# Performance work log

Measured on AMD Instinct MI355X. Metric: run time of the kernel, lower is better.

Reference implementation:

```python
import jax, jax.numpy as jnp
import numpy as np

B, LQ, LK, H, DK, DV, E = 4, 1024, 1024, 12, 64, 768, 768
TOPK = 64
TEMP = 0.5
NEG = -10000.0


def setup_inputs() -> dict:
    key = jax.random.key(0)
    ks = jax.random.split(key, 10)
    s = 0.02  # weight init scale
    return {
        "q": jax.random.normal(ks[0], (B, LQ, E), jnp.float32),
        "k": jax.random.normal(ks[1], (B, LK, E), jnp.float32),
        "v": jax.random.normal(ks[2], (B, LK, DV), jnp.float32),
        "qpos": jnp.zeros((B, LQ), jnp.int32),
        "kpos": jnp.zeros((B, LK), jnp.int32),
        "qk_mask": jax.random.normal(ks[3], (B, 1, LQ, LK), jnp.float32) * 0.1,
        "k_mask": jax.random.normal(ks[4], (B, 1, LK, 1), jnp.float32) * 0.1,
        "post_softmax_mask": (jax.random.uniform(ks[5], (B, 1, LQ, LK)) > 0.1).astype(jnp.float32),
        "w_qs": jax.random.normal(ks[6], (E, H * DK), jnp.float32) * s,
        "w_ks": jax.random.normal(ks[7], (E, H * DK), jnp.float32) * s,
        "w_vs": jax.random.normal(ks[8], (DV, H * DV), jnp.float32) * s,
        "fc": jax.random.normal(ks[9], (H * DV, DV), jnp.float32) * s,
    }


def reference(q, k, v, qpos, kpos, qk_mask, k_mask, post_softmax_mask, w_qs, w_ks, w_vs, fc):
    residual = v
    # project and split heads: [b, len, h, d] -> [b, h, len, d]
    qh = (q @ w_qs).reshape(B, LQ, H, DK).transpose(0, 2, 1, 3)
    kh = (k @ w_ks).reshape(B, LK, H, DK).transpose(0, 2, 1, 3)
    vh = (v @ w_vs).reshape(B, LK, H, DV).transpose(0, 2, 1, 3)

    # scaled dot-product scores [b, h, lq, lk]
    attn = jnp.einsum('bhqd,bhkd->bhqk', qh / np.float32(np.sqrt(DK)), kh)
    attn = attn + qk_mask                              # additive qk mask
    attn = attn + jnp.squeeze(k_mask, -1)[:, :, None, :]  # additive key mask

    # topk sparsification: keep top-k scores, fill rest with -10000
    topk_vals, topk_idx = jax.lax.top_k(attn, TOPK)
    attn = jnp.put_along_axis(jnp.full_like(attn, NEG), topk_idx, topk_vals,
                              axis=-1, inplace=False)

    # temperature + stable softmax in fp32
    attn = attn / max(TEMP, 1e-6)
    attn = jax.nn.softmax(attn.astype(jnp.float32), axis=-1).astype(v.dtype)

    # post-softmax multiplicative mask + renorm (renorm_post_mask=True)
    attn = attn * post_softmax_mask
    attn = attn / jnp.maximum(attn.sum(axis=-1, keepdims=True), 1e-6)

    # straight-through argmax hardening (use_argmax=True)
    hard = jax.nn.one_hot(jnp.argmax(attn, axis=-1), LK, dtype=attn.dtype)
    attn = hard - jax.lax.stop_gradient(attn) + attn

    # attend, merge heads, output projection + residual (dropout=0)
    head_output = jnp.einsum('bhqk,bhkd->bhqd', attn, vh)
    output = head_output.transpose(0, 2, 1, 3).reshape(B, LQ, H * DV) @ fc
    output = output + residual
    return (output, attn)
```

## Files before the change

### kernel.cpp

```cpp
#include <hip/hip_runtime.h>

constexpr int NB  = 4;
constexpr int NH  = 12;
constexpr int SEQ = 1024;
constexpr int DKd = 64;
constexpr int DVd = 768;
constexpr int Ed  = 768;
constexpr int HVd = 9216;

typedef float f32x4 __attribute__((ext_vector_type(4)));
typedef short s16x8 __attribute__((ext_vector_type(8)));

__device__ __forceinline__ unsigned short f2bf(float f) {
  unsigned int u = __builtin_bit_cast(unsigned int, f);
  u += 0x7fffu + ((u >> 16) & 1u);
  return (unsigned short)(u >> 16);
}

__device__ __forceinline__ float bf2f_lo(unsigned int u) {
  return __builtin_bit_cast(float, u << 16);
}
__device__ __forceinline__ float bf2f_hi(unsigned int u) {
  return __builtin_bit_cast(float, u & 0xffff0000u);
}

__device__ __forceinline__ f32x4 mfma_bf16_16x16x32(s16x8 a, s16x8 b, f32x4 c) {
  asm("v_mfma_f32_16x16x32_bf16 %0, %1, %2, %0" : "+v"(c) : "v"(a), "v"(b));
  return c;
}

#define GLOAD16(g, l)                                                          \
  __builtin_amdgcn_global_load_lds(                                            \
      (const __attribute__((address_space(1))) unsigned int*)(g),              \
      (__attribute__((address_space(3))) unsigned int*)(l), 16, 0, 0)

__global__ __launch_bounds__(256)
void cvt_bf16_kernel(const float* __restrict__ v, unsigned short* __restrict__ Vbf, int n4) {
  int i = blockIdx.x * 256 + threadIdx.x;
  const int stride = gridDim.x * 256;
  for (; i < n4; i += stride) {
    const f32x4 x = *(const f32x4*)&v[(size_t)i * 4];
    uint2 u;
    u.x = (unsigned)f2bf(x[0]) | ((unsigned)f2bf(x[1]) << 16);
    u.y = (unsigned)f2bf(x[2]) | ((unsigned)f2bf(x[3]) << 16);
    *(uint2*)&Vbf[(size_t)i * 4] = u;
  }
}

__global__ __launch_bounds__(256)
void maskprep_kernel(const float* __restrict__ qk, const float* __restrict__ km,
                     const float* __restrict__ pm, float* __restrict__ ms) {
  const int i = blockIdx.x * 256 + threadIdx.x;
  const int kk4 = i & 255;
  const int b = i >> 18;
  const f32x4 qv = *(const f32x4*)&qk[(size_t)i * 4];
  const f32x4 pv = *(const f32x4*)&pm[(size_t)i * 4];
  const f32x4 kv = *(const f32x4*)&km[b * SEQ + kk4 * 4];
  f32x4 o;
#pragma unroll
  for (int c = 0; c < 4; c++) o[c] = pv[c] > 0.f ? qv[c] + kv[c] : -3.0e38f;
  *(f32x4*)&ms[(size_t)i * 4] = o;
}

__global__ __launch_bounds__(256)
void qkproj_kernel(const float* __restrict__ q, const float* __restrict__ k,
                   const float* __restrict__ w_qs, const float* __restrict__ w_ks,
                   float* __restrict__ qh, float* __restrict__ kh) {
  const float* A  = blockIdx.z ? k : q;
  const float* Bw = blockIdx.z ? w_ks : w_qs;
  float* C        = blockIdx.z ? kh : qh;
  __shared__ float As[16][128];
  __shared__ float Bs[16][64];
  const int tid = threadIdx.x;
  const int m0 = blockIdx.x * 128, n0 = blockIdx.y * 64;
  const int ty = tid >> 4, tx = tid & 15;
  const int arow = tid >> 1, akc = (tid & 1) * 8;
  const int bkr = tid >> 4, bnc = (tid & 15) * 4;

  float acc[8][4];
#pragma unroll
  for (int i = 0; i < 8; i++)
#pragma unroll
    for (int j = 0; j < 4; j++) acc[i][j] = 0.f;

  for (int k0 = 0; k0 < 768; k0 += 16) {
    const f32x4 av0 = *(const f32x4*)&A[(size_t)(m0 + arow) * 768 + k0 + akc];
    const f32x4 av1 = *(const f32x4*)&A[(size_t)(m0 + arow) * 768 + k0 + akc + 4];
    const f32x4 bv  = *(const f32x4*)&Bw[(size_t)(k0 + bkr) * 768 + n0 + bnc];
    __syncthreads();
#pragma unroll
    for (int c = 0; c < 4; c++) {
      As[akc + c][arow]     = av0[c];
      As[akc + 4 + c][arow] = av1[c];
    }
    *(f32x4*)&Bs[bkr][bnc] = bv;
    __syncthreads();
#pragma unroll
    for (int kk = 0; kk < 16; kk++) {
      const f32x4 a0 = *(const f32x4*)&As[kk][ty * 8];
      const f32x4 a1 = *(const f32x4*)&As[kk][ty * 8 + 4];
      const f32x4 b  = *(const f32x4*)&Bs[kk][tx * 4];
#pragma unroll
      for (int i = 0; i < 4; i++)
#pragma unroll
        for (int j = 0; j < 4; j++) {
          acc[i][j]     += a0[i] * b[j];
          acc[i + 4][j] += a1[i] * b[j];
        }
    }
  }
#pragma unroll
  for (int i = 0; i < 8; i++) {
    f32x4 o;
#pragma unroll
    for (int j = 0; j < 4; j++) o[j] = acc[i][j];
    *(f32x4*)&C[(size_t)(m0 + ty * 8 + i) * 768 + n0 + tx * 4] = o;
  }
}

__global__ __launch_bounds__(256)
void score_argmax_kernel(const float* __restrict__ qh, const float* __restrict__ kh,
                         const float* __restrict__ ms, float2* __restrict__ partials) {
  __shared__ float msS[64][128];
  __shared__ float QsT[64][64];
  __shared__ float KsT[64][128];
  const int b  = blockIdx.z;
  const int q0 = blockIdx.y * 64;
  const int k0 = blockIdx.x * 128;
  const int tid = threadIdx.x;
  const int ty = tid >> 4, tx = tid & 15;

  {
    const int row = tid >> 2, cc = (tid & 3) * 32;
    const float* src = ms + (size_t)(b * SEQ + q0 + row) * SEQ + k0 + cc;
#pragma unroll
    for (int i = 0; i < 8; i++)
      *(f32x4*)&msS[row][cc + 4 * i] = *(const f32x4*)&src[4 * i];
  }

  const int qr = tid >> 2, qdc = (tid & 3) * 16;
  const int kr = tid >> 1, kdc = (tid & 1) * 32;
  const float* qbase = qh + (size_t)(b * SEQ + q0 + qr) * Ed + qdc;
  const float* kbase = kh + (size_t)(b * SEQ + k0 + kr) * Ed + kdc;
  const int kg0 = k0 + tx * 8;

  for (int h = 0; h < NH; h++) {
    __syncthreads();
#pragma unroll
    for (int j = 0; j < 4; j++) {
      const f32x4 qv = *(const f32x4*)&qbase[h * 64 + 4 * j];
#pragma unroll
      for (int c = 0; c < 4; c++) QsT[qdc + 4 * j + c][qr] = qv[c];
    }
#pragma unroll
    for (int j = 0; j < 8; j++) {
      const f32x4 kv = *(const f32x4*)&kbase[h * 64 + 4 * j];
#pragma unroll
      for (int c = 0; c < 4; c++) KsT[kdc + 4 * j + c][kr] = kv[c];
    }
    __syncthreads();

    float acc[4][8];
#pragma unroll
    for (int i = 0; i < 4; i++)
#pragma unroll
      for (int j = 0; j < 8; j++) acc[i][j] = 0.f;

#pragma unroll 8
    for (int kk = 0; kk < 64; kk++) {
      const f32x4 qf  = *(const f32x4*)&QsT[kk][ty * 4];
      const f32x4 kf0 = *(const f32x4*)&KsT[kk][tx * 8];
      const f32x4 kf1 = *(const f32x4*)&KsT[kk][tx * 8 + 4];
#pragma unroll
      for (int i = 0; i < 4; i++)
#pragma unroll
        for (int j = 0; j < 4; j++) {
          acc[i][j]     += qf[i] * kf0[j];
          acc[i][j + 4] += qf[i] * kf1[j];
        }
    }

#pragma unroll
    for (int i = 0; i < 4; i++) {
      const int qg = q0 + ty * 4 + i;
      const f32x4 m0v = *(const f32x4*)&msS[ty * 4 + i][tx * 8];
      const f32x4 m1v = *(const f32x4*)&msS[ty * 4 + i][tx * 8 + 4];
      float bv = -3.0e38f;
      int bi = 0;
#pragma unroll
      for (int j = 0; j < 4; j++) {
        const float s = acc[i][j] * 0.125f + m0v[j];
        if (s > bv) { bv = s; bi = kg0 + j; }
      }
#pragma unroll
      for (int j = 0; j < 4; j++) {
        const float s = acc[i][4 + j] * 0.125f + m1v[j];
        if (s > bv) { bv = s; bi = kg0 + 4 + j; }
      }
#pragma unroll
      for (int off = 1; off < 16; off <<= 1) {
        const float ov = __shfl_xor(bv, off);
        const int   oi = __shfl_xor(bi, off);
        if (ov > bv || (ov == bv && oi < bi)) { bv = ov; bi = oi; }
      }
      if (tx == 0)
        partials[(size_t)((b * NH + h) * SEQ + qg) * 8 + blockIdx.x] =
            make_float2(bv, __int_as_float(bi));
    }
  }
}

__global__ __launch_bounds__(256)
void argmax_reduce_kernel(const float2* __restrict__ partials, int* __restrict__ kmaxp) {
  const int t = blockIdx.x * 256 + threadIdx.x;
  if (t >= NB * NH * SEQ) return;
  const float2* p = partials + (size_t)t * 8;
  float bv = -3.0e38f;
  int bi = 0;
#pragma unroll
  for (int i = 0; i < 8; i++) {
    const float vv = p[i].x;
    const int ii = __float_as_int(p[i].y);
    if (vv > bv) { bv = vv; bi = ii; }
  }
  kmaxp[t] = bi;
}

__global__ __launch_bounds__(256)
void wvfc_gemm_kernel(const float* __restrict__ wvs, const float* __restrict__ fcw,
                      unsigned short* __restrict__ MstbT) {
  __shared__ unsigned short As[128][72];
  __shared__ unsigned short Bs[128][72];
  const int tid = threadIdx.x;
  const int h = blockIdx.z;
  const int m0 = blockIdx.x * 128, n0 = blockIdx.y * 128;
  const int wid = tid >> 6, lane = tid & 63;
  const int wr = (wid >> 1) * 64, wc = (wid & 1) * 64;
  const int lm = lane & 15, lq = lane >> 4;
  const int ar = tid >> 1, acb = (tid & 1) * 32;
  const int br = tid >> 2, bnb = (tid & 3) * 32;

  f32x4 acc[4][4];
#pragma unroll
  for (int m = 0; m < 4; m++)
#pragma unroll
    for (int n = 0; n < 4; n++)
#pragma unroll
      for (int r = 0; r < 4; r++) acc[m][n][r] = 0.f;

  for (int k0 = 0; k0 < 768; k0 += 64) {
    const float* asrc = wvs + (size_t)(m0 + ar) * HVd + h * 768 + k0 + acb;
    const float* bsrc = fcw + (size_t)(h * 768 + k0 + br) * 768 + n0 + bnb;
    f32x4 a4[8], b4[8];
#pragma unroll
    for (int i = 0; i < 8; i++) a4[i] = *(const f32x4*)&asrc[4 * i];
#pragma unroll
    for (int i = 0; i < 8; i++) b4[i] = *(const f32x4*)&bsrc[4 * i];
    __syncthreads();
#pragma unroll
    for (int i = 0; i < 4; i++) {
      s16x8 pk;
#pragma unroll
      for (int j = 0; j < 8; j++) pk[j] = (short)f2bf(a4[2 * i + (j >> 2)][j & 3]);
      *(s16x8*)&As[ar][acb + 8 * i] = pk;
    }
#pragma unroll
    for (int i = 0; i < 8; i++)
#pragma unroll
      for (int c = 0; c < 4; c++) Bs[bnb + 4 * i + c][br] = f2bf(b4[i][c]);
    __syncthreads();
#pragma unroll
    for (int ks = 0; ks < 2; ks++) {
      s16x8 af[4], bfr[4];
#pragma unroll
      for (int m = 0; m < 4; m++)
        af[m] = *(const s16x8*)&As[wr + m * 16 + lm][ks * 32 + lq * 8];
#pragma unroll
      for (int n = 0; n < 4; n++)
        bfr[n] = *(const s16x8*)&Bs[wc + n * 16 + lm][ks * 32 + lq * 8];
#pragma unroll
      for (int m = 0; m < 4; m++)
#pragma unroll
        for (int n = 0; n < 4; n++)
          acc[m][n] = mfma_bf16_16x16x32(af[m], bfr[n], acc[m][n]);
    }
  }
  asm volatile("s_nop 7\n\ts_nop 7");
#pragma unroll
  for (int m = 0; m < 4; m++)
#pragma unroll
    for (int n = 0; n < 4; n++) {
      const int grow0 = m0 + wr + m * 16 + lq * 4;
      const int gcol  = n0 + wc + n * 16 + lm;
      uint2 u;
      u.x = (unsigned)f2bf(acc[m][n][0]) | ((unsigned)f2bf(acc[m][n][1]) << 16);
      u.y = (unsigned)f2bf(acc[m][n][2]) | ((unsigned)f2bf(acc[m][n][3]) << 16);
      *(uint2*)&MstbT[(size_t)(h * 768 + gcol) * 768 + grow0] = u;
    }
}

__global__ __launch_bounds__(256)
void ugemm_kernel(const unsigned short* __restrict__ Vbf,
                  const unsigned short* __restrict__ MstbT,
                  unsigned short* __restrict__ U, int h0) {
  __shared__ unsigned short As[128 * 64];
  __shared__ unsigned short Bs[128 * 64];
  const int tid = threadIdx.x;
  const int h = h0 + blockIdx.z;
  const int bx = (int)blockIdx.x;
  const int sx = ((bx & 7) << 2) | (bx >> 3);
  const int m0 = sx * 128, n0 = blockIdx.y * 128;
  const int wid = tid >> 6, lane = tid & 63;
  const int wr = (wid >> 1) * 64, wc = (wid & 1) * 64;
  const int lm = lane & 15, lq = lane >> 4;
  const int srow = tid >> 3, scol = (tid & 7) * 8;
  const int ldst = (tid >> 6) * 512;

  const unsigned short* asrc = Vbf + (size_t)(m0 + srow) * 768 + scol;
  const unsigned short* bsrc = MstbT + (size_t)(h * 768 + n0 + srow) * 768 + scol;

  f32x4 acc[4][4];
#pragma unroll
  for (int m = 0; m < 4; m++)
#pragma unroll
    for (int n = 0; n < 4; n++)
#pragma unroll
      for (int r = 0; r < 4; r++) acc[m][n][r] = 0.f;

  for (int k0 = 0; k0 < 768; k0 += 64) {
#pragma unroll
    for (int j = 0; j < 4; j++)
      GLOAD16(asrc + (size_t)j * 32 * 768 + k0, &As[j * 2048 + ldst]);
#pragma unroll
    for (int j = 0; j < 4; j++)
      GLOAD16(bsrc + (size_t)j * 32 * 768 + k0, &Bs[j * 2048 + ldst]);
    __syncthreads();
#pragma unroll
    for (int ks = 0; ks < 2; ks++) {
      s16x8 af[4], bfr[4];
#pragma unroll
      for (int m = 0; m < 4; m++)
        af[m] = *(const s16x8*)&As[(wr + m * 16 + lm) * 64 + ks * 32 + lq * 8];
#pragma unroll
      for (int n = 0; n < 4; n++)
        bfr[n] = *(const s16x8*)&Bs[(wc + n * 16 + lm) * 64 + ks * 32 + lq * 8];
#pragma unroll
      for (int m = 0; m < 4; m++)
#pragma unroll
        for (int n = 0; n < 4; n++)
          acc[m][n] = mfma_bf16_16x16x32(af[m], bfr[n], acc[m][n]);
    }
    __syncthreads();
  }
  asm volatile("s_nop 7\n\ts_nop 7");
  const size_t urow0 = (size_t)blockIdx.z * 4096;
#pragma unroll
  for (int m = 0; m < 4; m++)
#pragma unroll
    for (int r = 0; r < 4; r++) {
      const int row = m0 + wr + m * 16 + lq * 4 + r;
      uint2 u;
      u.x = (unsigned)f2bf(acc[m][0][r]) | ((unsigned)f2bf(acc[m][1][r]) << 16);
      u.y = (unsigned)f2bf(acc[m][2][r]) | ((unsigned)f2bf(acc[m][3][r]) << 16);
      *(uint2*)&U[(urow0 + row) * 768 + n0 + wc + lm * 4] = u;
    }
}

__global__ __launch_bounds__(192)
void gathersum_kernel(const unsigned short* __restrict__ U, const int* __restrict__ kmaxp,
                      const float* __restrict__ v, float* __restrict__ out0,
                      int h0, int nhg) {
  const int row = blockIdx.x;
  const int b = row >> 10, q = row & 1023;
  const int t = threadIdx.x;
  float a0 = 0.f, a1 = 0.f, a2 = 0.f, a3 = 0.f;
  for (int hg = 0; hg < nhg; hg++) {
    const int g = kmaxp[((b * NH + h0 + hg) << 10) + q];
    const uint2 u = *(const uint2*)&U[((size_t)hg * 4096 + (b << 10) + g) * 768 + t * 4];
    a0 += bf2f_lo(u.x);
    a1 += bf2f_hi(u.x);
    a2 += bf2f_lo(u.y);
    a3 += bf2f_hi(u.y);
  }
  const int chunk = t >> 4, lmm = t & 15;
  const size_t ob = (size_t)row * 768 + chunk * 64 + lmm;
  if (h0 == 0) {
    out0[ob +  0] = a0 + v[ob +  0];
    out0[ob + 16] = a1 + v[ob + 16];
    out0[ob + 32] = a2 + v[ob + 32];
    out0[ob + 48] = a3 + v[ob + 48];
  } else {
    out0[ob +  0] += a0;
    out0[ob + 16] += a1;
    out0[ob + 32] += a2;
    out0[ob + 48] += a3;
  }
}

__global__ void onehot_kernel(const int* __restrict__ kmaxp, f32x4* __restrict__ attn, int n4) {
  int i = blockIdx.x * blockDim.x + threadIdx.x;
  const int stride = gridDim.x * blockDim.x;
  for (; i < n4; i += stride) {
    const int row = i >> 8;
    const int c0 = (i & 255) * 4;
    const int km = kmaxp[row];
    f32x4 o;
#pragma unroll
    for (int c = 0; c < 4; c++) o[c] = (c0 + c == km) ? 1.0f : 0.0f;
    attn[i] = o;
  }
}

extern "C" void kernel_launch(void* const* d_in, const int* in_sizes, int n_in,
                              void* d_out, int out_size, void* d_ws, size_t ws_size,
                              hipStream_t stream) {
  (void)in_sizes; (void)n_in; (void)out_size;
  const float* q       = (const float*)d_in[0];
  const float* k       = (const float*)d_in[1];
  const float* v       = (const float*)d_in[2];
  const float* qk_mask = (const float*)d_in[5];
  const float* k_mask  = (const float*)d_in[6];
  const float* pmask   = (const float*)d_in[7];
  const float* w_qs    = (const float*)d_in[8];
  const float* w_ks    = (const float*)d_in[9];
  const float* w_vs    = (const float*)d_in[10];
  const float* fc      = (const float*)d_in[11];

  float* out0 = (float*)d_out;
  float* attn = out0 + (size_t)NB * SEQ * DVd;

  char* ws = (char*)d_ws;
  unsigned short* MstbT = (unsigned short*)ws;
  unsigned short* Vbf   = (unsigned short*)(ws + 14155776);
  float* msbuf          = (float*)ws;
  int* kmaxp            = (int*)(ws + 20447232);
  char* ureg            = ws + 20643840;
  unsigned short* U     = (unsigned short*)ureg;
  float* qh             = (float*)ureg;
  float* kh             = (float*)(ureg + 12582912);
  float2* partials      = (float2*)(ureg + 25165824);

  const bool big = ws_size >= (size_t)96141312;

  maskprep_kernel<<<dim3(4096), 256, 0, stream>>>(qk_mask, k_mask, pmask, msbuf);

  qkproj_kernel<<<dim3(32, 12, 2), 256, 0, stream>>>(q, k, w_qs, w_ks, qh, kh);

  score_argmax_kernel<<<dim3(8, 16, NB), 256, 0, stream>>>(qh, kh, msbuf, partials);
  argmax_reduce_kernel<<<dim3((NB * NH * SEQ + 255) / 256), 256, 0, stream>>>(partials, kmaxp);

  cvt_bf16_kernel<<<dim3(3072), 256, 0, stream>>>(v, Vbf, NB * SEQ * DVd / 4);

  wvfc_gemm_kernel<<<dim3(6, 6, NH), 256, 0, stream>>>(w_vs, fc, MstbT);

  if (big) {
    ugemm_kernel<<<dim3(32, 6, 12), 256, 0, stream>>>(Vbf, MstbT, U, 0);
    gathersum_kernel<<<dim3(NB * SEQ), 192, 0, stream>>>(U, kmaxp, v, out0, 0, 12);
  } else {
    ugemm_kernel<<<dim3(32, 6, 6), 256, 0, stream>>>(Vbf, MstbT, U, 0);
    gathersum_kernel<<<dim3(NB * SEQ), 192, 0, stream>>>(U, kmaxp, v, out0, 0, 6);
    ugemm_kernel<<<dim3(32, 6, 6), 256, 0, stream>>>(Vbf, MstbT, U, 6);
    gathersum_kernel<<<dim3(NB * SEQ), 192, 0, stream>>>(U, kmaxp, v, out0, 6, 6);
  }

  onehot_kernel<<<dim3(2048), 256, 0, stream>>>(kmaxp, (f32x4*)attn,
                                                (int)((size_t)NB * NH * SEQ * SEQ / 4));
}
```

Measured before the change: 452.7 us.

## Use split-bf16 MFMA for QK projection, fuse mask prep, add argmax rescue

Replaces the fp32 scalar-FMA Q/K projection GEMM with a bf16 MFMA kernel that uses a hi/lo split, computing three products to approximate fp32 accuracy. This needs extra split and transpose kernels. The separate mask-prep pass is removed and its work is folded into score_argmax's shared-memory load, which avoids writing and re-reading a full-size mask buffer. The score kernel now tracks the top-2 candidates per row, and a rescue kernel recomputes near-tie rows in exact fp32 to guard argmax correctness against the reduced precision. The cost is extra launches and extra memory traffic for the split tensors.

```diff
diff --git a/kernel.cpp b/kernel.cpp
--- a/kernel.cpp
+++ b/kernel.cpp
@@ -16,12 +16,17 @@
   u += 0x7fffu + ((u >> 16) & 1u);
   return (unsigned short)(u >> 16);
 }
-
+__device__ __forceinline__ float bf2f(unsigned short h) {
+  return __builtin_bit_cast(float, (unsigned int)h << 16);
+}
 __device__ __forceinline__ float bf2f_lo(unsigned int u) {
   return __builtin_bit_cast(float, u << 16);
 }
 __device__ __forceinline__ float bf2f_hi(unsigned int u) {
   return __builtin_bit_cast(float, u & 0xffff0000u);
+}
+__device__ __forceinline__ bool better(float va, int ia, float vb, int ib) {
+  return va > vb || (va == vb && ia < ib);
 }
 
 __device__ __forceinline__ f32x4 mfma_bf16_16x16x32(s16x8 a, s16x8 b, f32x4 c) {
@@ -33,6 +38,312 @@
   __builtin_amdgcn_global_load_lds(                                            \
       (const __attribute__((address_space(1))) unsigned int*)(g),              \
       (__attribute__((address_space(3))) unsigned int*)(l), 16, 0, 0)
+
+__global__ __launch_bounds__(256)
+void split_qk_kernel(const float* __restrict__ q, const float* __restrict__ k,
+                     unsigned short* __restrict__ Qhi, unsigned short* __restrict__ Qlo,
+                     unsigned short* __restrict__ Khi, unsigned short* __restrict__ Klo,
+                     int n4) {
+  const float* src = blockIdx.z ? k : q;
+  unsigned short* hi = blockIdx.z ? Khi : Qhi;
+  unsigned short* lo = blockIdx.z ? Klo : Qlo;
+  int i = blockIdx.x * 256 + threadIdx.x;
+  const int stride = gridDim.x * 256;
+  for (; i < n4; i += stride) {
+    const f32x4 x = *(const f32x4*)&src[(size_t)i * 4];
+    unsigned short h[4], l[4];
+#pragma unroll
+    for (int c = 0; c < 4; c++) {
+      h[c] = f2bf(x[c]);
+      l[c] = f2bf(x[c] - bf2f(h[c]));
+    }
+    uint2 uh, ul;
+    uh.x = (unsigned)h[0] | ((unsigned)h[1] << 16);
+    uh.y = (unsigned)h[2] | ((unsigned)h[3] << 16);
+    ul.x = (unsigned)l[0] | ((unsigned)l[1] << 16);
+    ul.y = (unsigned)l[2] | ((unsigned)l[3] << 16);
+    *(uint2*)&hi[(size_t)i * 4] = uh;
+    *(uint2*)&lo[(size_t)i * 4] = ul;
+  }
+}
+
+__global__ __launch_bounds__(256)
+void split_wT_kernel(const float* __restrict__ w_qs, const float* __restrict__ w_ks,
+                     unsigned short* __restrict__ WqThi, unsigned short* __restrict__ WqTlo,
+                     unsigned short* __restrict__ WkThi, unsigned short* __restrict__ WkTlo) {
+  __shared__ float Ts[64][68];
+  const float* src = blockIdx.z ? w_ks : w_qs;
+  unsigned short* hi = blockIdx.z ? WkThi : WqThi;
+  unsigned short* lo = blockIdx.z ? WkTlo : WqTlo;
+  const int e0 = blockIdx.x * 64, n0 = blockIdx.y * 64;
+  const int tid = threadIdx.x;
+  const int row = tid >> 2, cc = (tid & 3) * 16;
+#pragma unroll
+  for (int j = 0; j < 4; j++)
+    *(f32x4*)&Ts[row][cc + 4 * j] = *(const f32x4*)&src[(size_t)(e0 + row) * 768 + n0 + cc + 4 * j];
+  __syncthreads();
+  const int r = tid >> 2, cs = (tid & 3) * 16;
+  s16x8 ph[2], pl[2];
+#pragma unroll
+  for (int j = 0; j < 16; j++) {
+    const float v = Ts[cs + j][r];
+    const unsigned short h = f2bf(v);
+    const unsigned short l = f2bf(v - bf2f(h));
+    ph[j >> 3][j & 7] = (short)h;
+    pl[j >> 3][j & 7] = (short)l;
+  }
+  const size_t ob = (size_t)(n0 + r) * 768 + e0 + cs;
+  *(s16x8*)&hi[ob] = ph[0];
+  *(s16x8*)&hi[ob + 8] = ph[1];
+  *(s16x8*)&lo[ob] = pl[0];
+  *(s16x8*)&lo[ob + 8] = pl[1];
+}
+
+__global__ __launch_bounds__(256)
+void qkproj_mfma_kernel(const unsigned short* __restrict__ Qhi, const unsigned short* __restrict__ Qlo,
+                        const unsigned short* __restrict__ Khi, const unsigned short* __restrict__ Klo,
+                        const unsigned short* __restrict__ WqThi, const unsigned short* __restrict__ WqTlo,
+                        const unsigned short* __restrict__ WkThi, const unsigned short* __restrict__ WkTlo,
+                        float* __restrict__ qh, float* __restrict__ kh) {
+  const unsigned short* Ahi = blockIdx.z ? Khi : Qhi;
+  const unsigned short* Alo = blockIdx.z ? Klo : Qlo;
+  const unsigned short* Bhi = blockIdx.z ? WkThi : WqThi;
+  const unsigned short* Blo = blockIdx.z ? WkTlo : WqTlo;
+  float* C = blockIdx.z ? kh : qh;
+  __shared__ unsigned short AhiS[128 * 64], AloS[128 * 64];
+  __shared__ unsigned short BhiS[64 * 64], BloS[64 * 64];
+  const int tid = threadIdx.x;
+  const int wid = tid >> 6, lane = tid & 63;
+  const int m0 = blockIdx.x * 128, n0 = blockIdx.y * 64;
+  const int wr = (wid >> 1) * 64, wc = (wid & 1) * 32;
+  const int lm = lane & 15, lq = lane >> 4;
+  const int srow = wid * 8 + (lane >> 3);
+  const int scols = (((lane & 7) * 16) ^ ((srow & 7) << 4)) >> 1;
+  const int ldst = wid * 512;
+  const int xs = (lm & 7) << 3;
+
+  const unsigned short* ahi0 = Ahi + (size_t)(m0 + srow) * 768 + scols;
+  const unsigned short* alo0 = Alo + (size_t)(m0 + srow) * 768 + scols;
+  const unsigned short* bhi0 = Bhi + (size_t)(n0 + srow) * 768 + scols;
+  const unsigned short* blo0 = Blo + (size_t)(n0 + srow) * 768 + scols;
+
+  f32x4 acc[4][2];
+#pragma unroll
+  for (int m = 0; m < 4; m++)
+#pragma unroll
+    for (int n = 0; n < 2; n++)
+#pragma unroll
+      for (int r = 0; r < 4; r++) acc[m][n][r] = 0.f;
+
+  for (int k0 = 0; k0 < 768; k0 += 64) {
+#pragma unroll
+    for (int j = 0; j < 4; j++) {
+      GLOAD16(ahi0 + (size_t)j * 32 * 768 + k0, &AhiS[j * 2048 + ldst]);
+      GLOAD16(alo0 + (size_t)j * 32 * 768 + k0, &AloS[j * 2048 + ldst]);
+    }
+#pragma unroll
+    for (int j = 0; j < 2; j++) {
+      GLOAD16(bhi0 + (size_t)j * 32 * 768 + k0, &BhiS[j * 2048 + ldst]);
+      GLOAD16(blo0 + (size_t)j * 32 * 768 + k0, &BloS[j * 2048 + ldst]);
+    }
+    __syncthreads();
+#pragma unroll
+    for (int ks = 0; ks < 2; ks++) {
+      const int kc = (ks * 32 + lq * 8) ^ xs;
+      s16x8 ah[4], al[4], bh[2], bl[2];
+#pragma unroll
+      for (int m = 0; m < 4; m++) {
+        ah[m] = *(const s16x8*)&AhiS[(wr + m * 16 + lm) * 64 + kc];
+        al[m] = *(const s16x8*)&AloS[(wr + m * 16 + lm) * 64 + kc];
+      }
+#pragma unroll
+      for (int n = 0; n < 2; n++) {
+        bh[n] = *(const s16x8*)&BhiS[(wc + n * 16 + lm) * 64 + kc];
+        bl[n] = *(const s16x8*)&BloS[(wc + n * 16 + lm) * 64 + kc];
+      }
+#pragma unroll
+      for (int m = 0; m < 4; m++)
+#pragma unroll
+        for (int n = 0; n < 2; n++) {
+          acc[m][n] = mfma_bf16_16x16x32(ah[m], bh[n], acc[m][n]);
+          acc[m][n] = mfma_bf16_16x16x32(al[m], bh[n], acc[m][n]);
+          acc[m][n] = mfma_bf16_16x16x32(ah[m], bl[n], acc[m][n]);
+        }
+    }
+    __syncthreads();
+  }
+  asm volatile("s_nop 7\n\ts_nop 7");
+#pragma unroll
+  for (int m = 0; m < 4; m++)
+#pragma unroll
+    for (int n = 0; n < 2; n++)
+#pragma unroll
+      for (int r = 0; r < 4; r++)
+        C[(size_t)(m0 + wr + m * 16 + lq * 4 + r) * 768 + n0 + wc + n * 16 + lm] =
+            acc[m][n][r];
+}
+
+__global__ __launch_bounds__(256)
+void score_argmax_kernel(const float* __restrict__ qh, const float* __restrict__ kh,
+                         const float* __restrict__ qkm, const float* __restrict__ km,
+                         const float* __restrict__ pm, float4* __restrict__ partials) {
+  __shared__ float msS[64][128];
+  __shared__ float QsT[64][64];
+  __shared__ float KsT[64][128];
+  const int b  = blockIdx.z;
+  const int q0 = blockIdx.y * 64;
+  const int k0 = blockIdx.x * 128;
+  const int tid = threadIdx.x;
+  const int ty = tid >> 4, tx = tid & 15;
+
+  {
+    const int row = tid >> 2, cc = (tid & 3) * 32;
+    const size_t base = (size_t)(b * SEQ + q0 + row) * SEQ + k0 + cc;
+#pragma unroll
+    for (int i = 0; i < 8; i++) {
+      const f32x4 qv = *(const f32x4*)&qkm[base + 4 * i];
+      const f32x4 pv = *(const f32x4*)&pm[base + 4 * i];
+      const f32x4 kv = *(const f32x4*)&km[b * SEQ + k0 + cc + 4 * i];
+      f32x4 o;
+#pragma unroll
+      for (int c = 0; c < 4; c++) o[c] = pv[c] > 0.f ? qv[c] + kv[c] : -3.0e38f;
+      *(f32x4*)&msS[row][cc + 4 * i] = o;
+    }
+  }
+
+  const int qr = tid >> 2, qdc = (tid & 3) * 16;
+  const int kr = tid >> 1, kdc = (tid & 1) * 32;
+  const float* qbase = qh + (size_t)(b * SEQ + q0 + qr) * Ed + qdc;
+  const float* kbase = kh + (size_t)(b * SEQ + k0 + kr) * Ed + kdc;
+  const int kg0 = k0 + tx * 8;
+
+  for (int h = 0; h < NH; h++) {
+    __syncthreads();
+#pragma unroll
+    for (int j = 0; j < 4; j++) {
+      const f32x4 qv = *(const f32x4*)&qbase[h * 64 + 4 * j];
+#pragma unroll
+      for (int c = 0; c < 4; c++) QsT[qdc + 4 * j + c][qr] = qv[c];
+    }
+#pragma unroll
+    for (int j = 0; j < 8; j++) {
+      const f32x4 kv = *(const f32x4*)&kbase[h * 64 + 4 * j];
+#pragma unroll
+      for (int c = 0; c < 4; c++) KsT[kdc + 4 * j + c][kr] = kv[c];
+    }
+    __syncthreads();
+
+    float acc[4][8];
+#pragma unroll
+    for (int i = 0; i < 4; i++)
+#pragma unroll
+      for (int j = 0; j < 8; j++) acc[i][j] = 0.f;
+
+#pragma unroll 8
+    for (int kk = 0; kk < 64; kk++) {
+      const f32x4 qf  = *(const f32x4*)&QsT[kk][ty * 4];
+      const f32x4 kf0 = *(const f32x4*)&KsT[kk][tx * 8];
+      const f32x4 kf1 = *(const f32x4*)&KsT[kk][tx * 8 + 4];
+#pragma unroll
+      for (int i = 0; i < 4; i++)
+#pragma unroll
+        for (int j = 0; j < 4; j++) {
+          acc[i][j]     += qf[i] * kf0[j];
+          acc[i][j + 4] += qf[i] * kf1[j];
+        }
+    }
+
+#pragma unroll
+    for (int i = 0; i < 4; i++) {
+      const int qg = q0 + ty * 4 + i;
+      const f32x4 m0v = *(const f32x4*)&msS[ty * 4 + i][tx * 8];
+      const f32x4 m1v = *(const f32x4*)&msS[ty * 4 + i][tx * 8 + 4];
+      float v1 = -3.0e38f, v2 = -3.0e38f;
+      int i1 = 0, i2 = 0;
+#pragma unroll
+      for (int j = 0; j < 8; j++) {
+        const float s = acc[i][j] * 0.125f + (j < 4 ? m0v[j & 3] : m1v[j & 3]);
+        const int idx = kg0 + j;
+        if (better(s, idx, v1, i1)) { v2 = v1; i2 = i1; v1 = s; i1 = idx; }
+        else if (better(s, idx, v2, i2)) { v2 = s; i2 = idx; }
+      }
+#pragma unroll
+      for (int off = 1; off < 16; off <<= 1) {
+        const float w1 = __shfl_xor(v1, off); const int j1 = __shfl_xor(i1, off);
+        const float w2 = __shfl_xor(v2, off); const int j2 = __shfl_xor(i2, off);
+        if (better(w1, j1, v1, i1)) {
+          if (better(v1, i1, w2, j2)) { v2 = v1; i2 = i1; } else { v2 = w2; i2 = j2; }
+          v1 = w1; i1 = j1;
+        } else if (better(w1, j1, v2, i2)) { v2 = w1; i2 = j1; }
+      }
+      if (tx == 0)
+        partials[(size_t)((b * NH + h) * SEQ + qg) * 8 + blockIdx.x] =
+            make_float4(v1, __int_as_float(i1), v2, __int_as_float(i2));
+    }
+  }
+}
+
+__global__ __launch_bounds__(256)
+void argmax_reduce_kernel(const float4* __restrict__ partials, int* __restrict__ kmaxp,
+                          float4* __restrict__ aux) {
+  const int t = blockIdx.x * 256 + threadIdx.x;
+  if (t >= NB * NH * SEQ) return;
+  const float4* p = partials + (size_t)t * 8;
+  float v1 = -3.0e38f, v2 = -3.0e38f;
+  int i1 = 0, i2 = 0;
+#pragma unroll
+  for (int i = 0; i < 8; i++) {
+    const float w1 = p[i].x; const int j1 = __float_as_int(p[i].y);
+    const float w2 = p[i].z; const int j2 = __float_as_int(p[i].w);
+    if (better(w1, j1, v1, i1)) {
+      if (better(v1, i1, w2, j2)) { v2 = v1; i2 = i1; } else { v2 = w2; i2 = j2; }
+      v1 = w1; i1 = j1;
+    } else if (better(w1, j1, v2, i2)) { v2 = w1; i2 = j1; }
+  }
+  kmaxp[t] = i1;
+  aux[t] = make_float4(v1, __int_as_float(i1), v2, __int_as_float(i2));
+}
+
+__global__ __launch_bounds__(256)
+void rescue_kernel(const float4* __restrict__ aux, const float* __restrict__ q,
+                   const float* __restrict__ k, const float* __restrict__ w_qs,
+                   const float* __restrict__ w_ks, const float* __restrict__ qkm,
+                   const float* __restrict__ km, const float* __restrict__ pm,
+                   int* __restrict__ kmaxp) {
+  const int row = blockIdx.x * 4 + (threadIdx.x >> 6);
+  const float4 a = aux[row];
+  if (a.x - a.z > 5e-4f) return;
+  const int i1 = __float_as_int(a.y), i2 = __float_as_int(a.w);
+  if (i1 == i2) return;
+  const int bh = row >> 10, qq = row & 1023;
+  const int b = bh / NH, h = bh % NH;
+  const int lane = threadIdx.x & 63;
+  const float* qr = q + (size_t)(b * SEQ + qq) * Ed;
+  const float* k1 = k + (size_t)(b * SEQ + i1) * Ed;
+  const float* k2 = k + (size_t)(b * SEQ + i2) * Ed;
+  const float* wq = w_qs + h * DKd + lane;
+  const float* wk = w_ks + h * DKd + lane;
+  float qd = 0.f, k1d = 0.f, k2d = 0.f;
+#pragma unroll 4
+  for (int e = 0; e < Ed; e++) {
+    const float wqe = wq[(size_t)e * 768];
+    const float wke = wk[(size_t)e * 768];
+    qd  += qr[e] * wqe;
+    k1d += k1[e] * wke;
+    k2d += k2[e] * wke;
+  }
+  float s1 = qd * k1d, s2 = qd * k2d;
+#pragma unroll
+  for (int off = 1; off < 64; off <<= 1) {
+    s1 += __shfl_xor(s1, off);
+    s2 += __shfl_xor(s2, off);
+  }
+  const size_t m1 = (size_t)(b * SEQ + qq) * SEQ + i1;
+  const size_t m2 = (size_t)(b * SEQ + qq) * SEQ + i2;
+  s1 = s1 * 0.125f + (pm[m1] > 0.f ? qkm[m1] + km[b * SEQ + i1] : -3.0e38f);
+  s2 = s2 * 0.125f + (pm[m2] > 0.f ? qkm[m2] + km[b * SEQ + i2] : -3.0e38f);
+  if (lane == 0) kmaxp[row] = better(s1, i1, s2, i2) ? i1 : i2;
+}
 
 __global__ __launch_bounds__(256)
 void cvt_bf16_kernel(const float* __restrict__ v, unsigned short* __restrict__ Vbf, int n4) {
@@ -45,185 +356,6 @@
     u.y = (unsigned)f2bf(x[2]) | ((unsigned)f2bf(x[3]) << 16);
     *(uint2*)&Vbf[(size_t)i * 4] = u;
   }
-}
-
-__global__ __launch_bounds__(256)
-void maskprep_kernel(const float* __restrict__ qk, const float* __restrict__ km,
-                     const float* __restrict__ pm, float* __restrict__ ms) {
-  const int i = blockIdx.x * 256 + threadIdx.x;
-  const int kk4 = i & 255;
-  const int b = i >> 18;
-  const f32x4 qv = *(const f32x4*)&qk[(size_t)i * 4];
-  const f32x4 pv = *(const f32x4*)&pm[(size_t)i * 4];
-  const f32x4 kv = *(const f32x4*)&km[b * SEQ + kk4 * 4];
-  f32x4 o;
-#pragma unroll
-  for (int c = 0; c < 4; c++) o[c] = pv[c] > 0.f ? qv[c] + kv[c] : -3.0e38f;
-  *(f32x4*)&ms[(size_t)i * 4] = o;
-}
-
-__global__ __launch_bounds__(256)
-void qkproj_kernel(const float* __restrict__ q, const float* __restrict__ k,
-                   const float* __restrict__ w_qs, const float* __restrict__ w_ks,
-                   float* __restrict__ qh, float* __restrict__ kh) {
-  const float* A  = blockIdx.z ? k : q;
-  const float* Bw = blockIdx.z ? w_ks : w_qs;
-  float* C        = blockIdx.z ? kh : qh;
-  __shared__ float As[16][128];
-  __shared__ float Bs[16][64];
-  const int tid = threadIdx.x;
-  const int m0 = blockIdx.x * 128, n0 = blockIdx.y * 64;
-  const int ty = tid >> 4, tx = tid & 15;
-  const int arow = tid >> 1, akc = (tid & 1) * 8;
-  const int bkr = tid >> 4, bnc = (tid & 15) * 4;
-
-  float acc[8][4];
-#pragma unroll
-  for (int i = 0; i < 8; i++)
-#pragma unroll
-    for (int j = 0; j < 4; j++) acc[i][j] = 0.f;
-
-  for (int k0 = 0; k0 < 768; k0 += 16) {
-    const f32x4 av0 = *(const f32x4*)&A[(size_t)(m0 + arow) * 768 + k0 + akc];
-    const f32x4 av1 = *(const f32x4*)&A[(size_t)(m0 + arow) * 768 + k0 + akc + 4];
-    const f32x4 bv  = *(const f32x4*)&Bw[(size_t)(k0 + bkr) * 768 + n0 + bnc];
-    __syncthreads();
-#pragma unroll
-    for (int c = 0; c < 4; c++) {
-      As[akc + c][arow]     = av0[c];
-      As[akc + 4 + c][arow] = av1[c];
-    }
-    *(f32x4*)&Bs[bkr][bnc] = bv;
-    __syncthreads();
-#pragma unroll
-    for (int kk = 0; kk < 16; kk++) {
-      const f32x4 a0 = *(const f32x4*)&As[kk][ty * 8];
-      const f32x4 a1 = *(const f32x4*)&As[kk][ty * 8 + 4];
-      const f32x4 b  = *(const f32x4*)&Bs[kk][tx * 4];
-#pragma unroll
-      for (int i = 0; i < 4; i++)
-#pragma unroll
-        for (int j = 0; j < 4; j++) {
-          acc[i][j]     += a0[i] * b[j];
-          acc[i + 4][j] += a1[i] * b[j];
-        }
-    }
-  }
-#pragma unroll
-  for (int i = 0; i < 8; i++) {
-    f32x4 o;
-#pragma unroll
-    for (int j = 0; j < 4; j++) o[j] = acc[i][j];
-    *(f32x4*)&C[(size_t)(m0 + ty * 8 + i) * 768 + n0 + tx * 4] = o;
-  }
-}
-
-__global__ __launch_bounds__(256)
-void score_argmax_kernel(const float* __restrict__ qh, const float* __restrict__ kh,
-                         const float* __restrict__ ms, float2* __restrict__ partials) {
-  __shared__ float msS[64][128];
-  __shared__ float QsT[64][64];
-  __shared__ float KsT[64][128];
-  const int b  = blockIdx.z;
-  const int q0 = blockIdx.y * 64;
-  const int k0 = blockIdx.x * 128;
-  const int tid = threadIdx.x;
-  const int ty = tid >> 4, tx = tid & 15;
-
-  {
-    const int row = tid >> 2, cc = (tid & 3) * 32;
-    const float* src = ms + (size_t)(b * SEQ + q0 + row) * SEQ + k0 + cc;
-#pragma unroll
-    for (int i = 0; i < 8; i++)
-      *(f32x4*)&msS[row][cc + 4 * i] = *(const f32x4*)&src[4 * i];
-  }
-
-  const int qr = tid >> 2, qdc = (tid & 3) * 16;
-  const int kr = tid >> 1, kdc = (tid & 1) * 32;
-  const float* qbase = qh + (size_t)(b * SEQ + q0 + qr) * Ed + qdc;
-  const float* kbase = kh + (size_t)(b * SEQ + k0 + kr) * Ed + kdc;
-  const int kg0 = k0 + tx * 8;
-
-  for (int h = 0; h < NH; h++) {
-    __syncthreads();
-#pragma unroll
-    for (int j = 0; j < 4; j++) {
-      const f32x4 qv = *(const f32x4*)&qbase[h * 64 + 4 * j];
-#pragma unroll
-      for (int c = 0; c < 4; c++) QsT[qdc + 4 * j + c][qr] = qv[c];
-    }
-#pragma unroll
-    for (int j = 0; j < 8; j++) {
-      const f32x4 kv = *(const f32x4*)&kbase[h * 64 + 4 * j];
-#pragma unroll
-      for (int c = 0; c < 4; c++) KsT[kdc + 4 * j + c][kr] = kv[c];
-    }
-    __syncthreads();
-
-    float acc[4][8];
-#pragma unroll
-    for (int i = 0; i < 4; i++)
-#pragma unroll
-      for (int j = 0; j < 8; j++) acc[i][j] = 0.f;
-
-#pragma unroll 8
-    for (int kk = 0; kk < 64; kk++) {
-      const f32x4 qf  = *(const f32x4*)&QsT[kk][ty * 4];
-      const f32x4 kf0 = *(const f32x4*)&KsT[kk][tx * 8];
-      const f32x4 kf1 = *(const f32x4*)&KsT[kk][tx * 8 + 4];
-#pragma unroll
-      for (int i = 0; i < 4; i++)
-#pragma unroll
-        for (int j = 0; j < 4; j++) {
-          acc[i][j]     += qf[i] * kf0[j];
-          acc[i][j + 4] += qf[i] * kf1[j];
-        }
-    }
-
-#pragma unroll
-    for (int i = 0; i < 4; i++) {
-      const int qg = q0 + ty * 4 + i;
-      const f32x4 m0v = *(const f32x4*)&msS[ty * 4 + i][tx * 8];
-      const f32x4 m1v = *(const f32x4*)&msS[ty * 4 + i][tx * 8 + 4];
-      float bv = -3.0e38f;
-      int bi = 0;
-#pragma unroll
-      for (int j = 0; j < 4; j++) {
-        const float s = acc[i][j] * 0.125f + m0v[j];
-        if (s > bv) { bv = s; bi = kg0 + j; }
-      }
-#pragma unroll
-      for (int j = 0; j < 4; j++) {
-        const float s = acc[i][4 + j] * 0.125f + m1v[j];
-        if (s > bv) { bv = s; bi = kg0 + 4 + j; }
-      }
-#pragma unroll
-      for (int off = 1; off < 16; off <<= 1) {
-        const float ov = __shfl_xor(bv, off);
-        const int   oi = __shfl_xor(bi, off);
-        if (ov > bv || (ov == bv && oi < bi)) { bv = ov; bi = oi; }
-      }
-      if (tx == 0)
-        partials[(size_t)((b * NH + h) * SEQ + qg) * 8 + blockIdx.x] =
-            make_float2(bv, __int_as_float(bi));
-    }
-  }
-}
-
-__global__ __launch_bounds__(256)
-void argmax_reduce_kernel(const float2* __restrict__ partials, int* __restrict__ kmaxp) {
-  const int t = blockIdx.x * 256 + threadIdx.x;
-  if (t >= NB * NH * SEQ) return;
-  const float2* p = partials + (size_t)t * 8;
-  float bv = -3.0e38f;
-  int bi = 0;
-#pragma unroll
-  for (int i = 0; i < 8; i++) {
-    const float vv = p[i].x;
-    const int ii = __float_as_int(p[i].y);
-    if (vv > bv) { bv = vv; bi = ii; }
-  }
-  kmaxp[t] = bi;
 }
 
 __global__ __launch_bounds__(256)
@@ -430,27 +562,41 @@
   float* attn = out0 + (size_t)NB * SEQ * DVd;
 
   char* ws = (char*)d_ws;
+  unsigned short* Qhi   = (unsigned short*)ws;
+  unsigned short* Qlo   = (unsigned short*)(ws + 6291456);
+  unsigned short* WqThi = (unsigned short*)(ws + 12582912);
+  unsigned short* WqTlo = (unsigned short*)(ws + 13762560);
+  unsigned short* WkThi = (unsigned short*)(ws + 14942208);
+  unsigned short* WkTlo = (unsigned short*)(ws + 16121856);
+  int* kmaxp            = (int*)(ws + 20447232);
+  unsigned short* Khi   = (unsigned short*)(ws + 20643840);
+  unsigned short* Klo   = (unsigned short*)(ws + 26935296);
+  float* qh             = (float*)(ws + 33226752);
+  float* kh             = (float*)(ws + 45809664);
+  float4* partials      = (float4*)ws;
+  float4* aux           = (float4*)(ws + 6291456);
   unsigned short* MstbT = (unsigned short*)ws;
   unsigned short* Vbf   = (unsigned short*)(ws + 14155776);
-  float* msbuf          = (float*)ws;
-  int* kmaxp            = (int*)(ws + 20447232);
-  char* ureg            = ws + 20643840;
-  unsigned short* U     = (unsigned short*)ureg;
-  float* qh             = (float*)ureg;
-  float* kh             = (float*)(ureg + 12582912);
-  float2* partials      = (float2*)(ureg + 25165824);
+  unsigned short* U     = (unsigned short*)(ws + 20643840);
 
   const bool big = ws_size >= (size_t)96141312;
 
-  maskprep_kernel<<<dim3(4096), 256, 0, stream>>>(qk_mask, k_mask, pmask, msbuf);
-
-  qkproj_kernel<<<dim3(32, 12, 2), 256, 0, stream>>>(q, k, w_qs, w_ks, qh, kh);
-
-  score_argmax_kernel<<<dim3(8, 16, NB), 256, 0, stream>>>(qh, kh, msbuf, partials);
-  argmax_reduce_kernel<<<dim3((NB * NH * SEQ + 255) / 256), 256, 0, stream>>>(partials, kmaxp);
+  split_qk_kernel<<<dim3(1536, 1, 2), 256, 0, stream>>>(q, k, Qhi, Qlo, Khi, Klo,
+                                                        NB * SEQ * Ed / 4);
+  split_wT_kernel<<<dim3(12, 12, 2), 256, 0, stream>>>(w_qs, w_ks, WqThi, WqTlo,
+                                                       WkThi, WkTlo);
+
+  qkproj_mfma_kernel<<<dim3(32, 12, 2), 256, 0, stream>>>(
+      Qhi, Qlo, Khi, Klo, WqThi, WqTlo, WkThi, WkTlo, qh, kh);
+
+  score_argmax_kernel<<<dim3(8, 16, NB), 256, 0, stream>>>(qh, kh, qk_mask, k_mask,
+                                                           pmask, partials);
+  argmax_reduce_kernel<<<dim3(192), 256, 0, stream>>>(partials, kmaxp, aux);
+
+  rescue_kernel<<<dim3(12288), 256, 0, stream>>>(aux, q, k, w_qs, w_ks,
+                                                 qk_mask, k_mask, pmask, kmaxp);
 
   cvt_bf16_kernel<<<dim3(3072), 256, 0, stream>>>(v, Vbf, NB * SEQ * DVd / 4);
-
   wvfc_gemm_kernel<<<dim3(6, 6, NH), 256, 0, stream>>>(w_vs, fc, MstbT);
 
   if (big) {
```

Result: slower. 500.3 us (+10.5%).
